# Performance work log

Measured on AMD Instinct MI355X. Metric: run time of the kernel, lower is better.

The kernel has to match this reference:

```python
import jax, jax.numpy as jnp
import numpy as np

ETA = 0.2  # temperature for expert reweighting
EPS = 1e-12  # F.normalize clamp


def setup_inputs() -> dict:
    key = jax.random.key(0)
    k1, k2, k3 = jax.random.split(key, 3)
    B, D_in, D, E = 8192, 1024, 512, 4
    x = jax.random.normal(k1, (B, D_in), dtype=jnp.float32)
    W = jax.random.normal(k2, (E, D_in, D), dtype=jnp.float32) * 0.02
    bias = jax.random.normal(k3, (E, D), dtype=jnp.float32) * 0.02
    return {"x": x, "W": W, "bias": bias}


def reference(x, W, bias):
    # expert logits: [E, B, D]
    logits = jnp.einsum('bi,eio->ebo', x, W) + bias[:, None, :]
    # F.normalize(dim=1): L2-normalize along class dim
    nrm = jnp.sqrt(jnp.sum(logits * logits, axis=-1, keepdims=True))
    xi = logits / jnp.maximum(nrm, EPS)  # [E, B, D]

    alpha = jnp.exp(xi) + 1.0
    S = jnp.sum(alpha, axis=-1, keepdims=True)      # [E, B, 1]
    bmass = (alpha - 1.0) / S                       # belief masses [E, B, D]
    d = xi.shape[-1]
    u = d / S[..., 0]                               # uncertainty [E, B]

    E, Bsz = xi.shape[0], xi.shape[1]
    ws = [jnp.ones((Bsz,), dtype=xi.dtype)]
    for i in range(E):
        if i == 0:
            C = jnp.zeros((Bsz,), dtype=xi.dtype)
        else:
            # conflict: sum_{j!=k} b0_j * b_k = (sum b0)(sum b) - <b0, b>
            b0, b1 = bmass[i - 1], bmass[i]
            C = jnp.sum(b0, -1) * jnp.sum(b1, -1) - jnp.sum(b0 * b1, -1)
        ws.append(ws[-1] * u[i] / (1.0 - C))

    # only ws[0..E-1] are used for reweighting (last append is unused)
    out = jnp.zeros_like(xi[0])
    for i in range(E):
        ew = jnp.exp(ws[i] / ETA)
        ew = ew / jnp.sum(ew)          # normalized over the BATCH, as in torch
        out = out + xi[i] * ew[:, None]
    return out
```

## Files before the change

kernel.cpp:

```cpp
#include <hip/hip_runtime.h>
#include <hip/hip_bf16.h>

#define BSZ   8192
#define DIN   1024
#define DOUT  512
#define NEXP  4

typedef __attribute__((ext_vector_type(8))) short short8;
typedef __attribute__((ext_vector_type(4))) float f32x4;

static __device__ inline unsigned short f32_to_bf16_rne(float f) {
    unsigned int u = __float_as_uint(f);
    unsigned int r = 0x7FFFu + ((u >> 16) & 1u);
    u += r;
    return (unsigned short)(u >> 16);
}

static __device__ inline float bf16_to_f32(unsigned short u) {
    return __uint_as_float(((unsigned int)u) << 16);
}

static __device__ inline float wred(float v) {
    for (int off = 1; off < 64; off <<= 1) v += __shfl_xor(v, off, 64);
    return v;
}

#define GLD_LDS16(g, l)                                                        \
    __builtin_amdgcn_global_load_lds(                                          \
        (const __attribute__((address_space(1))) void*)(g),                    \
        (__attribute__((address_space(3))) void*)(l), 16, 0, 0)

__global__ void convx_kernel(const float* __restrict__ x,
                             unsigned short* __restrict__ xb) {
    size_t i = ((size_t)blockIdx.x * 256 + threadIdx.x) * 8;
    float4 v0 = *(const float4*)&x[i];
    float4 v1 = *(const float4*)&x[i + 4];
    unsigned short tmp[8] = {
        f32_to_bf16_rne(v0.x), f32_to_bf16_rne(v0.y),
        f32_to_bf16_rne(v0.z), f32_to_bf16_rne(v0.w),
        f32_to_bf16_rne(v1.x), f32_to_bf16_rne(v1.y),
        f32_to_bf16_rne(v1.z), f32_to_bf16_rne(v1.w)};
    *(short8*)&xb[i] = *(short8*)tmp;
}

__global__ void convwt_kernel(const float* __restrict__ W,
                              unsigned short* __restrict__ Wt) {
    __shared__ float tile[32][33];
    int n0 = blockIdx.x * 32, k0 = blockIdx.y * 32, e = blockIdx.z;
    int c = threadIdx.x & 31, r4 = threadIdx.x >> 5;
    const float* Wp = W + ((size_t)e * DIN + k0) * DOUT + n0;
#pragma unroll
    for (int i = 0; i < 4; ++i) {
        int r = r4 + i * 8;
        tile[r][c] = Wp[(size_t)r * DOUT + c];
    }
    __syncthreads();
    unsigned short* Wtp = Wt + ((size_t)e * DOUT + n0) * DIN + k0;
#pragma unroll
    for (int i = 0; i < 4; ++i) {
        int r = r4 + i * 8;
        Wtp[(size_t)r * DIN + c] = f32_to_bf16_rne(tile[c][r]);
    }
}

__global__ __launch_bounds__(256) void gemm_kernel(
    const unsigned short* __restrict__ xb,
    const unsigned short* __restrict__ wtb,
    const float* __restrict__ bias,
    unsigned short* __restrict__ lgts) {
    __shared__ unsigned short As[128 * 32];
    __shared__ unsigned short Bs[128 * 32];
    const int tid = threadIdx.x;

    const int bid = blockIdx.x;
    const int swz = (bid & 7) * 128 + (bid >> 3);
    const int mt = swz >> 4;
    const int e  = (swz >> 2) & 3;
    const int nt = swz & 3;
    const int m0 = mt * 128;
    const int n0 = nt * 128;

    const unsigned short* Ag = xb + (size_t)m0 * DIN;
    const unsigned short* Bg = wtb + ((size_t)e * DOUT + n0) * DIN;

    const int lane = tid & 63, w = tid >> 6;
    const int wm = (w >> 1) * 64, wn = (w & 1) * 64;
    const int kk = (lane >> 4) * 8, rr = lane & 15;

    f32x4 acc[4][4] = {};

    const int f = tid;
    const int row0 = f >> 2, seg0 = f & 3;
    const int f1 = 256 + tid;
    const int row1 = f1 >> 2, seg1 = f1 & 3;

    for (int kt = 0; kt < DIN / 32; ++kt) {
        const int k0 = kt * 32;
        GLD_LDS16(Ag + (size_t)row0 * DIN + k0 + seg0 * 8, As + f * 8);
        GLD_LDS16(Bg + (size_t)row0 * DIN + k0 + seg0 * 8, Bs + f * 8);
        GLD_LDS16(Ag + (size_t)row1 * DIN + k0 + seg1 * 8, As + f1 * 8);
        GLD_LDS16(Bg + (size_t)row1 * DIN + k0 + seg1 * 8, Bs + f1 * 8);
        __syncthreads();

        short8 a[4], b[4];
#pragma unroll
        for (int i = 0; i < 4; ++i)
            a[i] = *(const short8*)&As[(wm + i * 16 + rr) * 32 + kk];
#pragma unroll
        for (int i = 0; i < 4; ++i)
            b[i] = *(const short8*)&Bs[(wn + i * 16 + rr) * 32 + kk];
#pragma unroll
        for (int i = 0; i < 4; ++i)
#pragma unroll
            for (int j = 0; j < 4; ++j)
                acc[i][j] = __builtin_amdgcn_mfma_f32_16x16x32_bf16(
                    a[i], b[j], acc[i][j], 0, 0, 0);
        __syncthreads();
    }

#pragma unroll
    for (int j = 0; j < 4; ++j) {
        const int gc = n0 + wn + j * 16 + rr;
        const float bv = bias[e * DOUT + gc];
#pragma unroll
        for (int i = 0; i < 4; ++i) {
            const int gr = m0 + wm + i * 16 + (lane >> 4) * 4;
            unsigned short* cp = lgts + ((size_t)e * BSZ + gr) * DOUT + gc;
#pragma unroll
            for (int r = 0; r < 4; ++r)
                cp[(size_t)r * DOUT] = f32_to_bf16_rne(acc[i][j][r] + bv);
        }
    }
}

__global__ __launch_bounds__(256) void rowstats_kernel(
    const unsigned short* __restrict__ lg,
    float4* __restrict__ rinv4, float4* __restrict__ ev4) {
    const int b = blockIdx.x * 4 + (threadIdx.x >> 6);
    const int lane = threadIdx.x & 63;

    float pe[8];
    float Tv[3], Pv[2], rinv[4];
#pragma unroll
    for (int e = 0; e < NEXP; ++e) {
        short8 v = *(const short8*)&lg[((size_t)e * BSZ + b) * DOUT + lane * 8];
        float l[8];
#pragma unroll
        for (int j = 0; j < 8; ++j) l[j] = bf16_to_f32((unsigned short)v[j]);
        float ss = 0.f;
#pragma unroll
        for (int j = 0; j < 8; ++j) ss += l[j] * l[j];
        ss = wred(ss);
        float ri = 1.0f / fmaxf(sqrtf(ss), 1e-12f);
        rinv[e] = ri;
        float t = 0.f, p = 0.f;
        float ce[8];
#pragma unroll
        for (int j = 0; j < 8; ++j) {
            ce[j] = expf(l[j] * ri);
            t += ce[j];
            if (e > 0) p += pe[j] * ce[j];
        }
        if (e < 3) Tv[e] = wred(t);
        if (e >= 1 && e <= 2) Pv[e - 1] = wred(p);
#pragma unroll
        for (int j = 0; j < 8; ++j) pe[j] = ce[j];
    }

    if (lane == 0) {
        const float d = (float)DOUT;
        float S0 = Tv[0] + d, S1 = Tv[1] + d, S2 = Tv[2] + d;
        float u0 = d / S0, u1 = d / S1, u2 = d / S2;
        float sb0 = Tv[0] / S0, sb1 = Tv[1] / S1, sb2 = Tv[2] / S2;
        float C1 = sb0 * sb1 - Pv[0] / (S0 * S1);
        float C2 = sb1 * sb2 - Pv[1] / (S1 * S2);
        float w1 = u0;
        float w2 = w1 * u1 / (1.0f - C1);
        float w3 = w2 * u2 / (1.0f - C2);
        ev4[b] = make_float4(expf(5.0f), expf(5.0f * w1), expf(5.0f * w2),
                             expf(5.0f * w3));
        rinv4[b] = make_float4(rinv[0], rinv[1], rinv[2], rinv[3]);
    }
}

__global__ __launch_bounds__(1024) void zred_kernel(
    const float4* __restrict__ ev4, float4* __restrict__ invZ) {
    __shared__ float4 sred[16];
    float4 s = make_float4(0.f, 0.f, 0.f, 0.f);
    for (int b = threadIdx.x; b < BSZ; b += 1024) {
        float4 v = ev4[b];
        s.x += v.x; s.y += v.y; s.z += v.z; s.w += v.w;
    }
    for (int off = 1; off < 64; off <<= 1) {
        s.x += __shfl_xor(s.x, off, 64);
        s.y += __shfl_xor(s.y, off, 64);
        s.z += __shfl_xor(s.z, off, 64);
        s.w += __shfl_xor(s.w, off, 64);
    }
    const int lane = threadIdx.x & 63, w = threadIdx.x >> 6;
    if (lane == 0) sred[w] = s;
    __syncthreads();
    if (threadIdx.x == 0) {
        float4 t = make_float4(0.f, 0.f, 0.f, 0.f);
#pragma unroll
        for (int i = 0; i < 16; ++i) {
            t.x += sred[i].x; t.y += sred[i].y;
            t.z += sred[i].z; t.w += sred[i].w;
        }
        invZ[0] = make_float4(1.f / t.x, 1.f / t.y, 1.f / t.z, 1.f / t.w);
    }
}

__global__ __launch_bounds__(256) void outk_kernel(
    const unsigned short* __restrict__ lg,
    const float4* __restrict__ rinv4, const float4* __restrict__ ev4,
    const float4* __restrict__ invZ, float* __restrict__ out) {
    const int b = blockIdx.x * 4 + (threadIdx.x >> 6);
    const int lane = threadIdx.x & 63;
    float4 iz = invZ[0];
    float4 ri = rinv4[b];
    float4 ev = ev4[b];
    float wgt[4] = {ev.x * iz.x * ri.x, ev.y * iz.y * ri.y,
                    ev.z * iz.z * ri.z, ev.w * iz.w * ri.w};
    float o[8] = {0.f, 0.f, 0.f, 0.f, 0.f, 0.f, 0.f, 0.f};
#pragma unroll
    for (int e = 0; e < NEXP; ++e) {
        short8 v = *(const short8*)&lg[((size_t)e * BSZ + b) * DOUT + lane * 8];
#pragma unroll
        for (int j = 0; j < 8; ++j)
            o[j] += bf16_to_f32((unsigned short)v[j]) * wgt[e];
    }
    float* op = out + (size_t)b * DOUT + lane * 8;
    *(float4*)op = make_float4(o[0], o[1], o[2], o[3]);
    *(float4*)(op + 4) = make_float4(o[4], o[5], o[6], o[7]);
}

extern "C" void kernel_launch(void* const* d_in, const int* in_sizes, int n_in,
                              void* d_out, int out_size, void* d_ws,
                              size_t ws_size, hipStream_t stream) {
    const float* x = (const float*)d_in[0];
    const float* W = (const float*)d_in[1];
    const float* bias = (const float*)d_in[2];
    float* out = (float*)d_out;

    char* ws = (char*)d_ws;
    unsigned short* lgts = (unsigned short*)ws;
    unsigned short* xb  = (unsigned short*)(ws + (size_t)33554432);
    unsigned short* wtb = (unsigned short*)(ws + (size_t)50331648);
    float4* rinv4 = (float4*)(ws + (size_t)54525952);
    float4* ev4   = (float4*)(ws + (size_t)54525952 + 131072);
    float4* invZ  = (float4*)(ws + (size_t)54525952 + 262144);

    convx_kernel<<<4096, 256, 0, stream>>>(x, xb);
    convwt_kernel<<<dim3(DOUT / 32, DIN / 32, NEXP), 256, 0, stream>>>(W, wtb);
    gemm_kernel<<<1024, 256, 0, stream>>>(xb, wtb, bias, lgts);
    rowstats_kernel<<<BSZ / 4, 256, 0, stream>>>(lgts, rinv4, ev4);
    zred_kernel<<<1, 1024, 0, stream>>>(ev4, invZ);
    outk_kernel<<<BSZ / 4, 256, 0, stream>>>(lgts, rinv4, ev4, invZ, out);
}
```

Baseline: 161.4 us.

## Double-buffer GEMM LDS tiles, merge conversion kernels, fold Z reduction into rowstats

The two conversion kernels become one prep kernel that dispatches on block index, and that kernel also zeroes the Z accumulator. The GEMM now double-buffers its LDS tiles, so the async global-to-LDS load of the next K tile is issued before computing the current one. The single-block Z reduction kernel is removed; rowstats does a per-block partial sum and adds it to Z with atomics. This cuts two launches and the serial single-block reduction, and hides load latency in the GEMM. In exchange it doubles LDS use, which may lower occupancy, and the float atomics make the summation order nondeterministic.

Measured after the change: 256.7 us. 59.1% more time.

```diff
diff --git a/kernel.cpp b/kernel.cpp
--- a/kernel.cpp
+++ b/kernel.cpp
@@ -30,36 +30,43 @@
         (const __attribute__((address_space(1))) void*)(g),                    \
         (__attribute__((address_space(3))) void*)(l), 16, 0, 0)
 
-__global__ void convx_kernel(const float* __restrict__ x,
-                             unsigned short* __restrict__ xb) {
-    size_t i = ((size_t)blockIdx.x * 256 + threadIdx.x) * 8;
-    float4 v0 = *(const float4*)&x[i];
-    float4 v1 = *(const float4*)&x[i + 4];
-    unsigned short tmp[8] = {
-        f32_to_bf16_rne(v0.x), f32_to_bf16_rne(v0.y),
-        f32_to_bf16_rne(v0.z), f32_to_bf16_rne(v0.w),
-        f32_to_bf16_rne(v1.x), f32_to_bf16_rne(v1.y),
-        f32_to_bf16_rne(v1.z), f32_to_bf16_rne(v1.w)};
-    *(short8*)&xb[i] = *(short8*)tmp;
-}
-
-__global__ void convwt_kernel(const float* __restrict__ W,
-                              unsigned short* __restrict__ Wt) {
+__global__ __launch_bounds__(256) void prep_kernel(
+    const float* __restrict__ x, const float* __restrict__ W,
+    unsigned short* __restrict__ xb, unsigned short* __restrict__ Wt,
+    float* __restrict__ Z) {
     __shared__ float tile[32][33];
-    int n0 = blockIdx.x * 32, k0 = blockIdx.y * 32, e = blockIdx.z;
-    int c = threadIdx.x & 31, r4 = threadIdx.x >> 5;
-    const float* Wp = W + ((size_t)e * DIN + k0) * DOUT + n0;
-#pragma unroll
-    for (int i = 0; i < 4; ++i) {
-        int r = r4 + i * 8;
-        tile[r][c] = Wp[(size_t)r * DOUT + c];
-    }
-    __syncthreads();
-    unsigned short* Wtp = Wt + ((size_t)e * DOUT + n0) * DIN + k0;
-#pragma unroll
-    for (int i = 0; i < 4; ++i) {
-        int r = r4 + i * 8;
-        Wtp[(size_t)r * DIN + c] = f32_to_bf16_rne(tile[c][r]);
+    const int bid = blockIdx.x;
+    if (bid < 4096) {
+        if (bid == 0 && threadIdx.x < 4) Z[threadIdx.x] = 0.0f;
+        size_t i = ((size_t)bid * 256 + threadIdx.x) * 8;
+        float4 v0 = *(const float4*)&x[i];
+        float4 v1 = *(const float4*)&x[i + 4];
+        unsigned short tmp[8] = {
+            f32_to_bf16_rne(v0.x), f32_to_bf16_rne(v0.y),
+            f32_to_bf16_rne(v0.z), f32_to_bf16_rne(v0.w),
+            f32_to_bf16_rne(v1.x), f32_to_bf16_rne(v1.y),
+            f32_to_bf16_rne(v1.z), f32_to_bf16_rne(v1.w)};
+        *(short8*)&xb[i] = *(short8*)tmp;
+    } else {
+        const int id = bid - 4096;
+        const int e = id >> 9;
+        const int rem = id & 511;
+        const int k0 = (rem >> 4) << 5;
+        const int n0 = (rem & 15) << 5;
+        const int c = threadIdx.x & 31, r4 = threadIdx.x >> 5;
+        const float* Wp = W + ((size_t)e * DIN + k0) * DOUT + n0;
+#pragma unroll
+        for (int i = 0; i < 4; ++i) {
+            int r = r4 + i * 8;
+            tile[r][c] = Wp[(size_t)r * DOUT + c];
+        }
+        __syncthreads();
+        unsigned short* Wtp = Wt + ((size_t)e * DOUT + n0) * DIN + k0;
+#pragma unroll
+        for (int i = 0; i < 4; ++i) {
+            int r = r4 + i * 8;
+            Wtp[(size_t)r * DIN + c] = f32_to_bf16_rne(tile[c][r]);
+        }
     }
 }
 
@@ -68,8 +75,8 @@
     const unsigned short* __restrict__ wtb,
     const float* __restrict__ bias,
     unsigned short* __restrict__ lgts) {
-    __shared__ unsigned short As[128 * 32];
-    __shared__ unsigned short Bs[128 * 32];
+    __shared__ unsigned short As[2][128 * 32];
+    __shared__ unsigned short Bs[2][128 * 32];
     const int tid = threadIdx.x;
 
     const int bid = blockIdx.x;
@@ -94,29 +101,41 @@
     const int f1 = 256 + tid;
     const int row1 = f1 >> 2, seg1 = f1 & 3;
 
-    for (int kt = 0; kt < DIN / 32; ++kt) {
-        const int k0 = kt * 32;
-        GLD_LDS16(Ag + (size_t)row0 * DIN + k0 + seg0 * 8, As + f * 8);
-        GLD_LDS16(Bg + (size_t)row0 * DIN + k0 + seg0 * 8, Bs + f * 8);
-        GLD_LDS16(Ag + (size_t)row1 * DIN + k0 + seg1 * 8, As + f1 * 8);
-        GLD_LDS16(Bg + (size_t)row1 * DIN + k0 + seg1 * 8, Bs + f1 * 8);
+#define STAGE(buf, kt)                                                         \
+    do {                                                                       \
+        const int k0_ = (kt) * 32;                                             \
+        GLD_LDS16(Ag + (size_t)row0 * DIN + k0_ + seg0 * 8, &As[buf][f * 8]);  \
+        GLD_LDS16(Bg + (size_t)row0 * DIN + k0_ + seg0 * 8, &Bs[buf][f * 8]);  \
+        GLD_LDS16(Ag + (size_t)row1 * DIN + k0_ + seg1 * 8, &As[buf][f1 * 8]); \
+        GLD_LDS16(Bg + (size_t)row1 * DIN + k0_ + seg1 * 8, &Bs[buf][f1 * 8]); \
+    } while (0)
+
+#define COMPUTE(buf)                                                           \
+    do {                                                                       \
+        short8 a[4], b[4];                                                     \
+        _Pragma("unroll") for (int i = 0; i < 4; ++i)                          \
+            a[i] = *(const short8*)&As[buf][(wm + i * 16 + rr) * 32 + kk];     \
+        _Pragma("unroll") for (int i = 0; i < 4; ++i)                          \
+            b[i] = *(const short8*)&Bs[buf][(wn + i * 16 + rr) * 32 + kk];     \
+        _Pragma("unroll") for (int i = 0; i < 4; ++i)                          \
+            _Pragma("unroll") for (int j = 0; j < 4; ++j)                      \
+                acc[i][j] = __builtin_amdgcn_mfma_f32_16x16x32_bf16(           \
+                    a[i], b[j], acc[i][j], 0, 0, 0);                           \
+    } while (0)
+
+    STAGE(0, 0);
+    __syncthreads();
+    int cur = 0;
+    for (int kt = 0; kt < DIN / 32 - 1; ++kt) {
+        STAGE(cur ^ 1, kt + 1);
+        COMPUTE(cur);
         __syncthreads();
-
-        short8 a[4], b[4];
-#pragma unroll
-        for (int i = 0; i < 4; ++i)
-            a[i] = *(const short8*)&As[(wm + i * 16 + rr) * 32 + kk];
-#pragma unroll
-        for (int i = 0; i < 4; ++i)
-            b[i] = *(const short8*)&Bs[(wn + i * 16 + rr) * 32 + kk];
-#pragma unroll
-        for (int i = 0; i < 4; ++i)
-#pragma unroll
-            for (int j = 0; j < 4; ++j)
-                acc[i][j] = __builtin_amdgcn_mfma_f32_16x16x32_bf16(
-                    a[i], b[j], acc[i][j], 0, 0, 0);
-        __syncthreads();
-    }
+        cur ^= 1;
+    }
+    COMPUTE(cur);
+
+#undef STAGE
+#undef COMPUTE
 
 #pragma unroll
     for (int j = 0; j < 4; ++j) {
@@ -135,8 +154,11 @@
 
 __global__ __launch_bounds__(256) void rowstats_kernel(
     const unsigned short* __restrict__ lg,
-    float4* __restrict__ rinv4, float4* __restrict__ ev4) {
-    const int b = blockIdx.x * 4 + (threadIdx.x >> 6);
+    float4* __restrict__ rinv4, float4* __restrict__ ev4,
+    float* __restrict__ Z) {
+    __shared__ float4 sz[4];
+    const int wv = threadIdx.x >> 6;
+    const int b = blockIdx.x * 4 + wv;
     const int lane = threadIdx.x & 63;
 
     float pe[8];
@@ -177,51 +199,36 @@
         float w1 = u0;
         float w2 = w1 * u1 / (1.0f - C1);
         float w3 = w2 * u2 / (1.0f - C2);
-        ev4[b] = make_float4(expf(5.0f), expf(5.0f * w1), expf(5.0f * w2),
-                             expf(5.0f * w3));
+        float4 ev = make_float4(expf(5.0f), expf(5.0f * w1), expf(5.0f * w2),
+                                expf(5.0f * w3));
+        ev4[b] = ev;
         rinv4[b] = make_float4(rinv[0], rinv[1], rinv[2], rinv[3]);
-    }
-}
-
-__global__ __launch_bounds__(1024) void zred_kernel(
-    const float4* __restrict__ ev4, float4* __restrict__ invZ) {
-    __shared__ float4 sred[16];
-    float4 s = make_float4(0.f, 0.f, 0.f, 0.f);
-    for (int b = threadIdx.x; b < BSZ; b += 1024) {
-        float4 v = ev4[b];
-        s.x += v.x; s.y += v.y; s.z += v.z; s.w += v.w;
-    }
-    for (int off = 1; off < 64; off <<= 1) {
-        s.x += __shfl_xor(s.x, off, 64);
-        s.y += __shfl_xor(s.y, off, 64);
-        s.z += __shfl_xor(s.z, off, 64);
-        s.w += __shfl_xor(s.w, off, 64);
-    }
-    const int lane = threadIdx.x & 63, w = threadIdx.x >> 6;
-    if (lane == 0) sred[w] = s;
+        sz[wv] = ev;
+    }
     __syncthreads();
     if (threadIdx.x == 0) {
-        float4 t = make_float4(0.f, 0.f, 0.f, 0.f);
-#pragma unroll
-        for (int i = 0; i < 16; ++i) {
-            t.x += sred[i].x; t.y += sred[i].y;
-            t.z += sred[i].z; t.w += sred[i].w;
-        }
-        invZ[0] = make_float4(1.f / t.x, 1.f / t.y, 1.f / t.z, 1.f / t.w);
+        float4 t = sz[0];
+        t.x += sz[1].x + sz[2].x + sz[3].x;
+        t.y += sz[1].y + sz[2].y + sz[3].y;
+        t.z += sz[1].z + sz[2].z + sz[3].z;
+        t.w += sz[1].w + sz[2].w + sz[3].w;
+        atomicAdd(&Z[0], t.x);
+        atomicAdd(&Z[1], t.y);
+        atomicAdd(&Z[2], t.z);
+        atomicAdd(&Z[3], t.w);
     }
 }
 
 __global__ __launch_bounds__(256) void outk_kernel(
     const unsigned short* __restrict__ lg,
     const float4* __restrict__ rinv4, const float4* __restrict__ ev4,
-    const float4* __restrict__ invZ, float* __restrict__ out) {
+    const float* __restrict__ Z, float* __restrict__ out) {
     const int b = blockIdx.x * 4 + (threadIdx.x >> 6);
     const int lane = threadIdx.x & 63;
-    float4 iz = invZ[0];
     float4 ri = rinv4[b];
     float4 ev = ev4[b];
-    float wgt[4] = {ev.x * iz.x * ri.x, ev.y * iz.y * ri.y,
-                    ev.z * iz.z * ri.z, ev.w * iz.w * ri.w};
+    float wgt[4] = {ev.x / Z[0] * ri.x, ev.y / Z[1] * ri.y,
+                    ev.z / Z[2] * ri.z, ev.w / Z[3] * ri.w};
     float o[8] = {0.f, 0.f, 0.f, 0.f, 0.f, 0.f, 0.f, 0.f};
 #pragma unroll
     for (int e = 0; e < NEXP; ++e) {
@@ -249,12 +256,10 @@
     unsigned short* wtb = (unsigned short*)(ws + (size_t)50331648);
     float4* rinv4 = (float4*)(ws + (size_t)54525952);
     float4* ev4   = (float4*)(ws + (size_t)54525952 + 131072);
-    float4* invZ  = (float4*)(ws + (size_t)54525952 + 262144);
-
-    convx_kernel<<<4096, 256, 0, stream>>>(x, xb);
-    convwt_kernel<<<dim3(DOUT / 32, DIN / 32, NEXP), 256, 0, stream>>>(W, wtb);
+    float*  Z     = (float*)(ws + (size_t)54525952 + 262144);
+
+    prep_kernel<<<6144, 256, 0, stream>>>(x, W, xb, wtb, Z);
     gemm_kernel<<<1024, 256, 0, stream>>>(xb, wtb, bias, lgts);
-    rowstats_kernel<<<BSZ / 4, 256, 0, stream>>>(lgts, rinv4, ev4);
-    zred_kernel<<<1, 1024, 0, stream>>>(ev4, invZ);
-    outk_kernel<<<BSZ / 4, 256, 0, stream>>>(lgts, rinv4, ev4, invZ, out);
-}
+    rowstats_kernel<<<BSZ / 4, 256, 0, stream>>>(lgts, rinv4, ev4, Z);
+    outk_kernel<<<BSZ / 4, 256, 0, stream>>>(lgts, rinv4, ev4, Z, out);
+}
```
